# Kernel tuning notes

Measured on AMD Instinct MI355X. Metric: run time of the kernel, lower is better.

The kernel has to match this reference:

```python
import jax, jax.numpy as jnp
import numpy as np

D_MODEL = 768
NUM_HEADS = 12
HEAD_DIM = D_MODEL // NUM_HEADS
B, S = 2, 2048


def setup_inputs() -> dict:
    key = jax.random.key(0)
    ks = jax.random.split(key, 12)
    s = 1.0 / np.sqrt(D_MODEL)
    inp = {
        "query": jax.random.normal(ks[0], (B, S, D_MODEL), jnp.float32),
        "key": jax.random.normal(ks[1], (B, S, D_MODEL), jnp.float32),
        "value": jax.random.normal(ks[2], (B, S, D_MODEL), jnp.float32),
        # causal mask; masked_fill(scores, mask == 0, -inf)
        "mask": jnp.tril(jnp.ones((S, S), jnp.int32))[None, None, :, :],
        "Wq": jax.random.uniform(ks[3], (D_MODEL, D_MODEL), jnp.float32, -s, s),
        "bq": jax.random.uniform(ks[4], (D_MODEL,), jnp.float32, -s, s),
        "Wk": jax.random.uniform(ks[5], (D_MODEL, D_MODEL), jnp.float32, -s, s),
        "bk": jax.random.uniform(ks[6], (D_MODEL,), jnp.float32, -s, s),
        "Wv": jax.random.uniform(ks[7], (D_MODEL, D_MODEL), jnp.float32, -s, s),
        "bv": jax.random.uniform(ks[8], (D_MODEL,), jnp.float32, -s, s),
        "Wo": jax.random.uniform(ks[9], (D_MODEL, D_MODEL), jnp.float32, -s, s),
        "bo": jax.random.uniform(ks[10], (D_MODEL,), jnp.float32, -s, s),
    }
    return inp


def reference(query, key, value, mask, Wq, bq, Wk, bk, Wv, bv, Wo, bo):
    Bq, Lq, Dm = query.shape
    Lk = key.shape[1]
    H, Dh = NUM_HEADS, HEAD_DIM
    # projections (torch Linear: x @ W.T + b), split into heads -> [B,H,L,Dh]
    q = (query @ Wq.T + bq).reshape(Bq, Lq, H, Dh).transpose(0, 2, 1, 3)
    k = (key @ Wk.T + bk).reshape(Bq, Lk, H, Dh).transpose(0, 2, 1, 3)
    v = (value @ Wv.T + bv).reshape(Bq, Lk, H, Dh).transpose(0, 2, 1, 3)
    scores = jnp.einsum("bhqd,bhkd->bhqk", q, k) / jnp.sqrt(jnp.float32(Dh))
    scores = jnp.where(mask == 0, -jnp.inf, scores)
    attn = jax.nn.softmax(scores, axis=-1)
    context = jnp.einsum("bhqk,bhkd->bhqd", attn, v)
    context = context.transpose(0, 2, 1, 3).reshape(Bq, Lq, Dm)
    return context @ Wo.T + bo
```

## Files before the change

kernel.cpp:

```cpp
#include <hip/hip_runtime.h>

#define DM    768
#define NH    12
#define NB    2
#define DHD   64
#define SQL   2048
#define MROWS 4096
#define WSZ   589824
#define XSZ   3145728
#define QSCALE 0.18033688f

typedef short  s16x8 __attribute__((ext_vector_type(8)));
typedef float  f32x4 __attribute__((ext_vector_type(4)));
typedef float  f32x16 __attribute__((ext_vector_type(16)));
typedef unsigned short u16x4 __attribute__((ext_vector_type(4)));
typedef unsigned short u16x8 __attribute__((ext_vector_type(8)));
typedef unsigned int   u32x4 __attribute__((ext_vector_type(4)));

static __device__ __forceinline__ unsigned short f2bf(float f) {
    unsigned int u = __builtin_bit_cast(unsigned int, f);
    u += 0x7FFFu + ((u >> 16) & 1u);
    return (unsigned short)(u >> 16);
}

static __device__ __forceinline__ unsigned int cvtpk1(float x, float y) {
    unsigned int r;
    asm("v_cvt_pk_bf16_f32 %0, %1, %2" : "=v"(r) : "v"(x), "v"(y));
    return r;
}

static __device__ __forceinline__ uint2 cvt2(float4 v) {
    return (uint2){cvtpk1(v.x, v.y), cvtpk1(v.z, v.w)};
}

static __device__ __forceinline__ f32x4 mfma16(s16x8 a, s16x8 b, f32x4 c) {
    return __builtin_amdgcn_mfma_f32_16x16x32_bf16(a, b, c, 0, 0, 0);
}
static __device__ __forceinline__ f32x16 mfma32(s16x8 a, s16x8 b, f32x16 c) {
    return __builtin_amdgcn_mfma_f32_32x32x16_bf16(a, b, c, 0, 0, 0);
}

__global__ __launch_bounds__(256)
void prep(const float* __restrict__ Xq, const float* __restrict__ Xk,
          const float* __restrict__ Xv,
          const float* __restrict__ Wq, const float* __restrict__ Wk,
          const float* __restrict__ Wv, const float* __restrict__ Wo,
          unsigned short* __restrict__ Xb, unsigned short* __restrict__ Wb)
{
    const int y = blockIdx.y;
    const float* src;
    unsigned short* dst;
    int nv;
    if (y < 3) {
        src = (y == 0) ? Xq : (y == 1) ? Xk : Xv;
        dst = Xb + (size_t)y * XSZ;
        nv = XSZ / 8;
    } else {
        const int z = y - 3;
        src = (z == 0) ? Wq : (z == 1) ? Wk : (z == 2) ? Wv : Wo;
        dst = Wb + (size_t)z * WSZ;
        nv = WSZ / 8;
    }
    for (int i = blockIdx.x * 256 + threadIdx.x; i < nv; i += gridDim.x * 256) {
        float4 a = *reinterpret_cast<const float4*>(&src[(size_t)i * 8]);
        float4 b = *reinterpret_cast<const float4*>(&src[(size_t)i * 8 + 4]);
        uint2 p0 = cvt2(a), p1 = cvt2(b);
        u32x4 pk = {p0.x, p0.y, p1.x, p1.y};
        *reinterpret_cast<u32x4*>(&dst[(size_t)i * 8]) = pk;
    }
}

__global__ __launch_bounds__(256)
void qkv_proj(const unsigned short* __restrict__ Xb,
              const unsigned short* __restrict__ Wb,
              const float* __restrict__ bq, const float* __restrict__ bk,
              const float* __restrict__ bv,
              unsigned short* __restrict__ Qo, unsigned short* __restrict__ Ko,
              unsigned short* __restrict__ Vo)
{
    const int z = blockIdx.z;
    const unsigned short* X = Xb + (size_t)z * XSZ;
    const unsigned short* W = Wb + (size_t)z * WSZ;
    const float* bias = (z == 0) ? bq : (z == 1) ? bk : bv;
    unsigned short* O = (z == 0) ? Qo : (z == 1) ? Ko : Vo;

    __shared__ unsigned short As[64][72];
    __shared__ unsigned short Bs[128][72];

    const int tid  = threadIdx.x;
    const int lane = tid & 63;
    const int w    = tid >> 6;
    const int wm   = w >> 1, wn = w & 1;
    const int l15  = lane & 15, lg = lane >> 4;
    const int m0   = blockIdx.y * 64;
    const int n0   = blockIdx.x * 128;
    const int ar   = tid >> 2, ac = (tid & 3) << 4;
    const int br   = tid >> 1, bc = (tid & 1) << 5;

    f32x4 acc[2][4];
    #pragma unroll
    for (int i = 0; i < 2; ++i)
        #pragma unroll
        for (int j = 0; j < 4; ++j)
            acc[i][j] = (f32x4){0.f, 0.f, 0.f, 0.f};

    u16x8 ra[2], rb[4];
    #pragma unroll
    for (int i = 0; i < 2; ++i)
        ra[i] = *reinterpret_cast<const u16x8*>(&X[(size_t)(m0 + ar) * DM + ac + i * 8]);
    #pragma unroll
    for (int i = 0; i < 4; ++i)
        rb[i] = *reinterpret_cast<const u16x8*>(&W[(size_t)(n0 + br) * DM + bc + i * 8]);
    #pragma unroll
    for (int i = 0; i < 2; ++i)
        *reinterpret_cast<u16x8*>(&As[ar][ac + i * 8]) = ra[i];
    #pragma unroll
    for (int i = 0; i < 4; ++i)
        *reinterpret_cast<u16x8*>(&Bs[br][bc + i * 8]) = rb[i];
    __syncthreads();

    for (int k0 = 0; k0 < DM; k0 += 64) {
        const bool more = (k0 + 64 < DM);
        if (more) {
            #pragma unroll
            for (int i = 0; i < 2; ++i)
                ra[i] = *reinterpret_cast<const u16x8*>(&X[(size_t)(m0 + ar) * DM + k0 + 64 + ac + i * 8]);
            #pragma unroll
            for (int i = 0; i < 4; ++i)
                rb[i] = *reinterpret_cast<const u16x8*>(&W[(size_t)(n0 + br) * DM + k0 + 64 + bc + i * 8]);
        }
        s16x8 af[2][2], bfg[4][2];
        #pragma unroll
        for (int mi = 0; mi < 2; ++mi)
            #pragma unroll
            for (int ks = 0; ks < 2; ++ks)
                af[mi][ks] = *reinterpret_cast<const s16x8*>(&As[wm * 32 + mi * 16 + l15][ks * 32 + lg * 8]);
        #pragma unroll
        for (int nj = 0; nj < 4; ++nj)
            #pragma unroll
            for (int ks = 0; ks < 2; ++ks)
                bfg[nj][ks] = *reinterpret_cast<const s16x8*>(&Bs[wn * 64 + nj * 16 + l15][ks * 32 + lg * 8]);
        #pragma unroll
        for (int mi = 0; mi < 2; ++mi)
            #pragma unroll
            for (int nj = 0; nj < 4; ++nj)
                #pragma unroll
                for (int ks = 0; ks < 2; ++ks)
                    acc[mi][nj] = mfma16(af[mi][ks], bfg[nj][ks], acc[mi][nj]);
        __syncthreads();
        if (more) {
            #pragma unroll
            for (int i = 0; i < 2; ++i)
                *reinterpret_cast<u16x8*>(&As[ar][ac + i * 8]) = ra[i];
            #pragma unroll
            for (int i = 0; i < 4; ++i)
                *reinterpret_cast<u16x8*>(&Bs[br][bc + i * 8]) = rb[i];
            __syncthreads();
        }
    }

    const float scale = (z == 0) ? QSCALE : 1.0f;
    #pragma unroll
    for (int mi = 0; mi < 2; ++mi) {
        #pragma unroll
        for (int nj = 0; nj < 4; ++nj) {
            int col = n0 + wn * 64 + nj * 16 + l15;
            float bb = bias[col];
            int hh = col >> 6, d = col & 63;
            if (z < 2) {
                #pragma unroll
                for (int r = 0; r < 4; ++r) {
                    int row = m0 + wm * 32 + mi * 16 + (lg << 2) + r;
                    int b = row >> 11, s = row & (SQL - 1);
                    O[(((size_t)(b * NH + hh) * SQL) + s) * DHD + d] =
                        f2bf((acc[mi][nj][r] + bb) * scale);
                }
            } else {
                int row = m0 + wm * 32 + mi * 16 + (lg << 2);
                int b = row >> 11, s = row & (SQL - 1);
                u16x4 pk;
                #pragma unroll
                for (int r = 0; r < 4; ++r) pk[r] = f2bf(acc[mi][nj][r] + bb);
                *reinterpret_cast<u16x4*>(&O[(((size_t)(b * NH + hh) * DHD) + d) * SQL + s]) = pk;
            }
        }
    }
}

__global__ __launch_bounds__(512)
void attn(const unsigned short* __restrict__ Q, const unsigned short* __restrict__ K,
          const unsigned short* __restrict__ Vt, unsigned short* __restrict__ Ctx)
{
    __shared__ float Acc[8][2112];

    const int tid  = threadIdx.x;
    const int lane = tid & 63;
    const int w    = tid >> 6;
    const int hi   = lane >> 5;
    const int l31  = lane & 31;
    const int q0   = (gridDim.x - 1 - blockIdx.x) * 32;
    const int bh   = blockIdx.y;

    const unsigned short* Qb = Q  + (size_t)bh * SQL * DHD;
    const unsigned short* Kb = K  + (size_t)bh * SQL * DHD;
    const unsigned short* Vb = Vt + (size_t)bh * DHD * SQL;

    s16x8 qf[4];
    #pragma unroll
    for (int t = 0; t < 4; ++t)
        qf[t] = *reinterpret_cast<const s16x8*>(&Qb[(size_t)(q0 + l31) * DHD + t * 16 + hi * 8]);

    f32x16 o0 = {}, o1 = {};
    float m = -__builtin_inff(), l = 0.f;
    const int nkt = (q0 >> 5) + 1;

    int cnt = (w < nkt) ? ((nkt - w + 7) >> 3) : 0;
    int kt  = w;

    while (cnt >= 2) {
        const int ka = kt * 32, kb2 = (kt + 8) * 32;

        s16x8 kfa[4], kfb[4];
        #pragma unroll
        for (int t = 0; t < 4; ++t) {
            kfa[t] = *reinterpret_cast<const s16x8*>(&Kb[(size_t)(ka + l31) * DHD + t * 16 + hi * 8]);
            kfb[t] = *reinterpret_cast<const s16x8*>(&Kb[(size_t)(kb2 + l31) * DHD + t * 16 + hi * 8]);
        }
        s16x8 va00 = *reinterpret_cast<const s16x8*>(&Vb[(size_t)(l31)      * SQL + ka + hi * 8]);
        s16x8 va01 = *reinterpret_cast<const s16x8*>(&Vb[(size_t)(l31)      * SQL + ka + 16 + hi * 8]);
        s16x8 va10 = *reinterpret_cast<const s16x8*>(&Vb[(size_t)(32 + l31) * SQL + ka + hi * 8]);
        s16x8 va11 = *reinterpret_cast<const s16x8*>(&Vb[(size_t)(32 + l31) * SQL + ka + 16 + hi * 8]);
        s16x8 vb00 = *reinterpret_cast<const s16x8*>(&Vb[(size_t)(l31)      * SQL + kb2 + hi * 8]);
        s16x8 vb01 = *reinterpret_cast<const s16x8*>(&Vb[(size_t)(l31)      * SQL + kb2 + 16 + hi * 8]);
        s16x8 vb10 = *reinterpret_cast<const s16x8*>(&Vb[(size_t)(32 + l31) * SQL + kb2 + hi * 8]);
        s16x8 vb11 = *reinterpret_cast<const s16x8*>(&Vb[(size_t)(32 + l31) * SQL + kb2 + 16 + hi * 8]);

        f32x16 sa = {}, sb = {};
        #pragma unroll
        for (int t = 0; t < 4; ++t) sa = mfma32(kfa[t], qf[t], sa);
        #pragma unroll
        for (int t = 0; t < 4; ++t) sb = mfma32(kfb[t], qf[t], sb);

        if (kt + 8 == nkt - 1) {
            #pragma unroll
            for (int r = 0; r < 16; ++r) {
                int kvr = (r & 3) + 8 * (r >> 2) + 4 * hi;
                if (kvr > l31) sb[r] = -1.0e30f;
            }
        }

        float pm = fmaxf(sa[0], sb[0]);
        #pragma unroll
        for (int r = 1; r < 16; ++r) pm = fmaxf(pm, fmaxf(sa[r], sb[r]));
        pm = fmaxf(pm, __shfl_xor(pm, 32));
        const float mn = fmaxf(m, pm);
        const float al = __builtin_amdgcn_exp2f(m - mn);
        m = mn;

        float rs = 0.f;
        #pragma unroll
        for (int r = 0; r < 16; ++r) {
            sa[r] = __builtin_amdgcn_exp2f(sa[r] - mn); rs += sa[r];
            sb[r] = __builtin_amdgcn_exp2f(sb[r] - mn); rs += sb[r];
        }
        rs += __shfl_xor(rs, 32);
        l = l * al + rs;

        #pragma unroll
        for (int r = 0; r < 16; ++r) { o0[r] *= al; o1[r] *= al; }

        s16x8 pfa[2], pfb[2];
        #pragma unroll
        for (int ks = 0; ks < 2; ++ks) {
            const int rb = ks * 8;
            unsigned int a0 = cvtpk1(sa[rb + 0], sa[rb + 1]);
            unsigned int b0 = cvtpk1(sa[rb + 4], sa[rb + 5]);
            asm("v_permlane32_swap_b32 %0, %1" : "+v"(a0), "+v"(b0));
            unsigned int a1 = cvtpk1(sa[rb + 2], sa[rb + 3]);
            unsigned int b1 = cvtpk1(sa[rb + 6], sa[rb + 7]);
            asm("v_permlane32_swap_b32 %0, %1" : "+v"(a1), "+v"(b1));
            u32x4 pw = {a0, a1, b0, b1};
            pfa[ks] = __builtin_bit_cast(s16x8, pw);
        }
        #pragma unroll
        for (int ks = 0; ks < 2; ++ks) {
            const int rb = ks * 8;
            unsigned int a0 = cvtpk1(sb[rb + 0], sb[rb + 1]);
            unsigned int b0 = cvtpk1(sb[rb + 4], sb[rb + 5]);
            asm("v_permlane32_swap_b32 %0, %1" : "+v"(a0), "+v"(b0));
            unsigned int a1 = cvtpk1(sb[rb + 2], sb[rb + 3]);
            unsigned int b1 = cvtpk1(sb[rb + 6], sb[rb + 7]);
            asm("v_permlane32_swap_b32 %0, %1" : "+v"(a1), "+v"(b1));
            u32x4 pw = {a0, a1, b0, b1};
            pfb[ks] = __builtin_bit_cast(s16x8, pw);
        }

        o0 = mfma32(va00, pfa[0], o0);
        o0 = mfma32(va01, pfa[1], o0);
        o1 = mfma32(va10, pfa[0], o1);
        o1 = mfma32(va11, pfa[1], o1);
        o0 = mfma32(vb00, pfb[0], o0);
        o0 = mfma32(vb01, pfb[1], o0);
        o1 = mfma32(vb10, pfb[0], o1);
        o1 = mfma32(vb11, pfb[1], o1);

        kt += 16; cnt -= 2;
    }

    if (cnt) {
        const int ka = kt * 32;
        s16x8 kfa[4];
        #pragma unroll
        for (int t = 0; t < 4; ++t)
            kfa[t] = *reinterpret_cast<const s16x8*>(&Kb[(size_t)(ka + l31) * DHD + t * 16 + hi * 8]);
        s16x8 va00 = *reinterpret_cast<const s16x8*>(&Vb[(size_t)(l31)      * SQL + ka + hi * 8]);
        s16x8 va01 = *reinterpret_cast<const s16x8*>(&Vb[(size_t)(l31)      * SQL + ka + 16 + hi * 8]);
        s16x8 va10 = *reinterpret_cast<const s16x8*>(&Vb[(size_t)(32 + l31) * SQL + ka + hi * 8]);
        s16x8 va11 = *reinterpret_cast<const s16x8*>(&Vb[(size_t)(32 + l31) * SQL + ka + 16 + hi * 8]);

        f32x16 sa = {};
        #pragma unroll
        for (int t = 0; t < 4; ++t) sa = mfma32(kfa[t], qf[t], sa);

        if (kt == nkt - 1) {
            #pragma unroll
            for (int r = 0; r < 16; ++r) {
                int kvr = (r & 3) + 8 * (r >> 2) + 4 * hi;
                if (kvr > l31) sa[r] = -1.0e30f;
            }
        }

        float pm = sa[0];
        #pragma unroll
        for (int r = 1; r < 16; ++r) pm = fmaxf(pm, sa[r]);
        pm = fmaxf(pm, __shfl_xor(pm, 32));
        const float mn = fmaxf(m, pm);
        const float al = __builtin_amdgcn_exp2f(m - mn);
        m = mn;

        float rs = 0.f;
        #pragma unroll
        for (int r = 0; r < 16; ++r) {
            sa[r] = __builtin_amdgcn_exp2f(sa[r] - mn); rs += sa[r];
        }
        rs += __shfl_xor(rs, 32);
        l = l * al + rs;

        #pragma unroll
        for (int r = 0; r < 16; ++r) { o0[r] *= al; o1[r] *= al; }

        s16x8 pfa[2];
        #pragma unroll
        for (int ks = 0; ks < 2; ++ks) {
            const int rb = ks * 8;
            unsigned int a0 = cvtpk1(sa[rb + 0], sa[rb + 1]);
            unsigned int b0 = cvtpk1(sa[rb + 4], sa[rb + 5]);
            asm("v_permlane32_swap_b32 %0, %1" : "+v"(a0), "+v"(b0));
            unsigned int a1 = cvtpk1(sa[rb + 2], sa[rb + 3]);
            unsigned int b1 = cvtpk1(sa[rb + 6], sa[rb + 7]);
            asm("v_permlane32_swap_b32 %0, %1" : "+v"(a1), "+v"(b1));
            u32x4 pw = {a0, a1, b0, b1};
            pfa[ks] = __builtin_bit_cast(s16x8, pw);
        }

        o0 = mfma32(va00, pfa[0], o0);
        o0 = mfma32(va01, pfa[1], o0);
        o1 = mfma32(va10, pfa[0], o1);
        o1 = mfma32(va11, pfa[1], o1);
    }

    #pragma unroll
    for (int r = 0; r < 16; ++r) {
        int d = (r & 3) + 8 * (r >> 2) + 4 * hi;
        Acc[w][d * 32 + l31]        = o0[r];
        Acc[w][(32 + d) * 32 + l31] = o1[r];
    }
    if (hi == 0) { Acc[w][2048 + l31] = m; Acc[w][2080 + l31] = l; }
    __syncthreads();

    {
        const int q  = tid & 31;
        const int d4 = (tid >> 5) << 2;
        float M = -__builtin_inff();
        float mv[8];
        #pragma unroll
        for (int j = 0; j < 8; ++j) { mv[j] = Acc[j][2048 + q]; M = fmaxf(M, mv[j]); }
        float f[8]; float L = 0.f;
        #pragma unroll
        for (int j = 0; j < 8; ++j) {
            f[j] = __builtin_amdgcn_exp2f(mv[j] - M);
            L += f[j] * Acc[j][2080 + q];
        }
        const float invL = 1.0f / L;
        const int b = bh / NH, h = bh % NH;
        u16x4 pk;
        #pragma unroll
        for (int jj = 0; jj < 4; ++jj) {
            int d = d4 + jj;
            float o = 0.f;
            #pragma unroll
            for (int j = 0; j < 8; ++j) o += f[j] * Acc[j][d * 32 + q];
            pk[jj] = f2bf(o * invL);
        }
        *reinterpret_cast<u16x4*>(&Ctx[(((size_t)(b * SQL + q0 + q) * NH) + h) * DHD + d4]) = pk;
    }
}

__global__ __launch_bounds__(256)
void out_proj(const unsigned short* __restrict__ Ctx, const unsigned short* __restrict__ Wob,
              const float* __restrict__ bo, float* __restrict__ Out)
{
    __shared__ unsigned short As[64][72];
    __shared__ unsigned short Bs[64][72];

    const int tid  = threadIdx.x;
    const int lane = tid & 63;
    const int w    = tid >> 6;
    const int wm   = w >> 1, wn = w & 1;
    const int l15  = lane & 15, lg = lane >> 4;
    const int m0   = blockIdx.y * 64;
    const int n0   = blockIdx.x * 64;
    const int ar   = tid >> 2, ac = (tid & 3) << 4;

    f32x4 acc[2][2];
    #pragma unroll
    for (int i = 0; i < 2; ++i)
        #pragma unroll
        for (int j = 0; j < 2; ++j)
            acc[i][j] = (f32x4){0.f, 0.f, 0.f, 0.f};

    u16x8 ra[2], rb[2];
    #pragma unroll
    for (int i = 0; i < 2; ++i) {
        ra[i] = *reinterpret_cast<const u16x8*>(&Ctx[(size_t)(m0 + ar) * DM + ac + i * 8]);
        rb[i] = *reinterpret_cast<const u16x8*>(&Wob[(size_t)(n0 + ar) * DM + ac + i * 8]);
    }
    #pragma unroll
    for (int i = 0; i < 2; ++i) {
        *reinterpret_cast<u16x8*>(&As[ar][ac + i * 8]) = ra[i];
        *reinterpret_cast<u16x8*>(&Bs[ar][ac + i * 8]) = rb[i];
    }
    __syncthreads();

    for (int k0 = 0; k0 < DM; k0 += 64) {
        const bool more = (k0 + 64 < DM);
        if (more) {
            #pragma unroll
            for (int i = 0; i < 2; ++i) {
                ra[i] = *reinterpret_cast<const u16x8*>(&Ctx[(size_t)(m0 + ar) * DM + k0 + 64 + ac + i * 8]);
                rb[i] = *reinterpret_cast<const u16x8*>(&Wob[(size_t)(n0 + ar) * DM + k0 + 64 + ac + i * 8]);
            }
        }
        s16x8 af[2][2], bfg[2][2];
        #pragma unroll
        for (int mi = 0; mi < 2; ++mi)
            #pragma unroll
            for (int ks = 0; ks < 2; ++ks) {
                af[mi][ks]  = *reinterpret_cast<const s16x8*>(&As[wm * 32 + mi * 16 + l15][ks * 32 + lg * 8]);
                bfg[mi][ks] = *reinterpret_cast<const s16x8*>(&Bs[wn * 32 + mi * 16 + l15][ks * 32 + lg * 8]);
            }
        #pragma unroll
        for (int mi = 0; mi < 2; ++mi)
            #pragma unroll
            for (int nj = 0; nj < 2; ++nj)
                #pragma unroll
                for (int ks = 0; ks < 2; ++ks)
                    acc[mi][nj] = mfma16(af[mi][ks], bfg[nj][ks], acc[mi][nj]);
        __syncthreads();
        if (more) {
            #pragma unroll
            for (int i = 0; i < 2; ++i) {
                *reinterpret_cast<u16x8*>(&As[ar][ac + i * 8]) = ra[i];
                *reinterpret_cast<u16x8*>(&Bs[ar][ac + i * 8]) = rb[i];
            }
            __syncthreads();
        }
    }

    #pragma unroll
    for (int mi = 0; mi < 2; ++mi)
        #pragma unroll
        for (int nj = 0; nj < 2; ++nj) {
            int col = n0 + wn * 32 + nj * 16 + l15;
            float bb = bo[col];
            #pragma unroll
            for (int r = 0; r < 4; ++r) {
                int row = m0 + wm * 32 + mi * 16 + (lg << 2) + r;
                Out[(size_t)row * DM + col] = acc[mi][nj][r] + bb;
            }
        }
}

extern "C" void kernel_launch(void* const* d_in, const int* in_sizes, int n_in,
                              void* d_out, int out_size, void* d_ws, size_t ws_size,
                              hipStream_t stream) {
    const float* query = (const float*)d_in[0];
    const float* key   = (const float*)d_in[1];
    const float* value = (const float*)d_in[2];
    const float* Wq = (const float*)d_in[4];
    const float* bq = (const float*)d_in[5];
    const float* Wk = (const float*)d_in[6];
    const float* bk = (const float*)d_in[7];
    const float* Wv = (const float*)d_in[8];
    const float* bv = (const float*)d_in[9];
    const float* Wo = (const float*)d_in[10];
    const float* bo = (const float*)d_in[11];
    float* out = (float*)d_out;

    unsigned short* Wb  = (unsigned short*)d_ws;
    unsigned short* Xb  = Wb  + (size_t)4 * WSZ;
    unsigned short* Qb  = Xb  + (size_t)3 * XSZ;
    unsigned short* Kb  = Qb  + (size_t)XSZ;
    unsigned short* Vtb = Kb  + (size_t)XSZ;
    unsigned short* Ctx = Xb;

    prep<<<dim3(384, 7), 256, 0, stream>>>(query, key, value, Wq, Wk, Wv, Wo, Xb, Wb);
    qkv_proj<<<dim3(6, 64, 3), 256, 0, stream>>>(Xb, Wb, bq, bk, bv, Qb, Kb, Vtb);
    attn<<<dim3(64, NB * NH), 512, 0, stream>>>(Qb, Kb, Vtb, Ctx);
    out_proj<<<dim3(12, 64), 256, 0, stream>>>(Ctx, Wb + (size_t)3 * WSZ, bo, out);
}
```

Measured before the change: 248.9 us.

## Enlarge QKV projection tile to 128x128 and remap attention blocks per XCD

The QKV projection kernel now uses 512 threads and a 128x128 output tile, so each B tile loaded into shared memory serves twice as many rows and fewer blocks are launched. Separately, the attention grid is flattened to 1D and block ids are mapped so that each XCD (block id mod 8) handles three fixed (batch, head) pairs, keeping each head's K/V resident in one XCD's L2. The reversed query-tile order is preserved so the longest causal tiles start first. Risks are lower occupancy from the larger GEMM blocks, and a remapping that hardcodes 24 heads across 8 XCDs.

```diff
diff --git a/kernel.cpp b/kernel.cpp
--- a/kernel.cpp
+++ b/kernel.cpp
@@ -70,7 +70,7 @@
     }
 }
 
-__global__ __launch_bounds__(256)
+__global__ __launch_bounds__(512)
 void qkv_proj(const unsigned short* __restrict__ Xb,
               const unsigned short* __restrict__ Wb,
               const float* __restrict__ bq, const float* __restrict__ bk,
@@ -84,7 +84,7 @@
     const float* bias = (z == 0) ? bq : (z == 1) ? bk : bv;
     unsigned short* O = (z == 0) ? Qo : (z == 1) ? Ko : Vo;
 
-    __shared__ unsigned short As[64][72];
+    __shared__ unsigned short As[128][72];
     __shared__ unsigned short Bs[128][72];
 
     const int tid  = threadIdx.x;
@@ -92,10 +92,9 @@
     const int w    = tid >> 6;
     const int wm   = w >> 1, wn = w & 1;
     const int l15  = lane & 15, lg = lane >> 4;
-    const int m0   = blockIdx.y * 64;
+    const int m0   = blockIdx.y * 128;
     const int n0   = blockIdx.x * 128;
     const int ar   = tid >> 2, ac = (tid & 3) << 4;
-    const int br   = tid >> 1, bc = (tid & 1) << 5;
 
     f32x4 acc[2][4];
     #pragma unroll
@@ -104,30 +103,27 @@
         for (int j = 0; j < 4; ++j)
             acc[i][j] = (f32x4){0.f, 0.f, 0.f, 0.f};
 
-    u16x8 ra[2], rb[4];
-    #pragma unroll
-    for (int i = 0; i < 2; ++i)
+    u16x8 ra[2], rb[2];
+    #pragma unroll
+    for (int i = 0; i < 2; ++i) {
         ra[i] = *reinterpret_cast<const u16x8*>(&X[(size_t)(m0 + ar) * DM + ac + i * 8]);
-    #pragma unroll
-    for (int i = 0; i < 4; ++i)
-        rb[i] = *reinterpret_cast<const u16x8*>(&W[(size_t)(n0 + br) * DM + bc + i * 8]);
-    #pragma unroll
-    for (int i = 0; i < 2; ++i)
+        rb[i] = *reinterpret_cast<const u16x8*>(&W[(size_t)(n0 + ar) * DM + ac + i * 8]);
+    }
+    #pragma unroll
+    for (int i = 0; i < 2; ++i) {
         *reinterpret_cast<u16x8*>(&As[ar][ac + i * 8]) = ra[i];
-    #pragma unroll
-    for (int i = 0; i < 4; ++i)
-        *reinterpret_cast<u16x8*>(&Bs[br][bc + i * 8]) = rb[i];
+        *reinterpret_cast<u16x8*>(&Bs[ar][ac + i * 8]) = rb[i];
+    }
     __syncthreads();
 
     for (int k0 = 0; k0 < DM; k0 += 64) {
         const bool more = (k0 + 64 < DM);
         if (more) {
             #pragma unroll
-            for (int i = 0; i < 2; ++i)
+            for (int i = 0; i < 2; ++i) {
                 ra[i] = *reinterpret_cast<const u16x8*>(&X[(size_t)(m0 + ar) * DM + k0 + 64 + ac + i * 8]);
-            #pragma unroll
-            for (int i = 0; i < 4; ++i)
-                rb[i] = *reinterpret_cast<const u16x8*>(&W[(size_t)(n0 + br) * DM + k0 + 64 + bc + i * 8]);
+                rb[i] = *reinterpret_cast<const u16x8*>(&W[(size_t)(n0 + ar) * DM + k0 + 64 + ac + i * 8]);
+            }
         }
         s16x8 af[2][2], bfg[4][2];
         #pragma unroll
@@ -150,11 +146,10 @@
         __syncthreads();
         if (more) {
             #pragma unroll
-            for (int i = 0; i < 2; ++i)
+            for (int i = 0; i < 2; ++i) {
                 *reinterpret_cast<u16x8*>(&As[ar][ac + i * 8]) = ra[i];
-            #pragma unroll
-            for (int i = 0; i < 4; ++i)
-                *reinterpret_cast<u16x8*>(&Bs[br][bc + i * 8]) = rb[i];
+                *reinterpret_cast<u16x8*>(&Bs[ar][ac + i * 8]) = rb[i];
+            }
             __syncthreads();
         }
     }
@@ -198,8 +193,13 @@
     const int w    = tid >> 6;
     const int hi   = lane >> 5;
     const int l31  = lane & 31;
-    const int q0   = (gridDim.x - 1 - blockIdx.x) * 32;
-    const int bh   = blockIdx.y;
+
+    const int id  = blockIdx.x;
+    const int xcd = id & 7;
+    const int rr  = id >> 3;
+    const int bh  = xcd * 3 + (rr % 3);
+    const int qt  = 63 - rr / 3;
+    const int q0  = qt * 32;
 
     const unsigned short* Qb = Q  + (size_t)bh * SQL * DHD;
     const unsigned short* Kb = K  + (size_t)bh * SQL * DHD;
@@ -515,7 +515,7 @@
     unsigned short* Ctx = Xb;
 
     prep<<<dim3(384, 7), 256, 0, stream>>>(query, key, value, Wq, Wk, Wv, Wo, Xb, Wb);
-    qkv_proj<<<dim3(6, 64, 3), 256, 0, stream>>>(Xb, Wb, bq, bk, bv, Qb, Kb, Vtb);
-    attn<<<dim3(64, NB * NH), 512, 0, stream>>>(Qb, Kb, Vtb, Ctx);
+    qkv_proj<<<dim3(6, 32, 3), 512, 0, stream>>>(Xb, Wb, bq, bk, bv, Qb, Kb, Vtb);
+    attn<<<dim3(NB * NH * 64), 512, 0, stream>>>(Qb, Kb, Vtb, Ctx);
     out_proj<<<dim3(12, 64), 256, 0, stream>>>(Ctx, Wb + (size_t)3 * WSZ, bo, out);
 }
```

Result: faster. 220.5 us (-11.4%).
